# Kernel optimization log

Hardware: AMD Instinct MI355X
Metric: run time of the kernel (lower is better)

The kernel has to match this reference:

```python
import jax, jax.numpy as jnp
import numpy as np

B, H, L, D = 1, 8, 2048, 64
DP = 3   # positional coord dim
RE = 1   # extra relative features appended via concat
F = DP + RE  # LazyLinear in-features


def setup_inputs() -> dict:
    key = jax.random.key(0)
    ks = jax.random.split(key, 12)
    return {
        "q": jax.random.normal(ks[0], (B, H, L, D), jnp.float32),
        "k": jax.random.normal(ks[1], (B, H, L, D), jnp.float32),
        "v": jax.random.normal(ks[2], (B, H, L, D), jnp.float32),
        "c": jax.random.uniform(ks[3], (B, 1, 1, L), jnp.float32),
        "d_q": jax.random.normal(ks[4], (B, L, DP), jnp.float32),
        "d_k_top": jax.random.normal(ks[5], (B, L, DP), jnp.float32),
        "d_k_bot": jax.random.normal(ks[6], (B, L, DP), jnp.float32),
        "d_k_score": jax.random.uniform(ks[7], (B, L, 2, F), jnp.float32),
        "relative_top": jax.random.normal(ks[8], (B, L, L, RE), jnp.float32),
        "relative_bottom": jax.random.normal(ks[9], (B, L, L, RE), jnp.float32),
        "W_w": jax.random.normal(ks[10], (F, H), jnp.float32) * 0.1,
        "W_b": jax.random.normal(ks[11], (F, H), jnp.float32) * 0.1,
    }


def _pairwise_diff(a, b):
    # a: [B,Lq,Dp], b: [B,Lk,Dp] -> [B,Lq,Lk,Dp]
    return a[:, :, None, :] - b[:, None, :, :]


def reference(q, k, v, c, d_q, d_k_top, d_k_bot, d_k_score,
              relative_top, relative_bottom, W_w, W_b):
    # score function: scaled dot product -> [B,H,Lq,Lk]
    scores = jnp.einsum('bhqd,bhkd->bhqk', q, k) * (q.shape[-1] ** -0.5)

    # relative-position bias path
    dt = jnp.concatenate([_pairwise_diff(d_q, d_k_top), relative_top], axis=-1)     # [B,Lq,Lk,F]
    db = jnp.concatenate([_pairwise_diff(d_q, d_k_bot), relative_bottom], axis=-1)  # [B,Lq,Lk,F]
    dm = jnp.stack([dt, db], axis=3)                 # [B,Lq,Lk,2,F]
    dm = dm * d_k_score[:, None]                     # broadcast over Lq
    dm = dm.sum(axis=3)                              # [B,Lq,Lk,F]

    w = jax.nn.softplus(dm @ W_w).transpose(0, 3, 1, 2)  # [B,H,Lq,Lk]
    b = (dm @ W_b).transpose(0, 3, 1, 2)                 # [B,H,Lq,Lk]
    scores = scores * w + b

    # leaky probability function: softmax gated by per-key sampling weights c
    probs = jax.nn.softmax(scores, axis=-1) * c      # [B,H,Lq,Lk]

    out = jnp.einsum('bhqk,bhkd->bhqd', probs, v)
    return out, probs
```

## Files before the change

### kernel.cpp

```cpp
#include <hip/hip_runtime.h>
#include <cstdint>
#include <cstddef>

#define NH 8
#define LQ 2048
#define DH 64
#define NKT_HALF 16

typedef __attribute__((ext_vector_type(8))) __bf16 bf16x8;
typedef __attribute__((ext_vector_type(8))) unsigned short ushort8;
typedef __attribute__((ext_vector_type(4))) float floatx4;

__device__ __forceinline__ unsigned short bf_trunc(float x) {
    return (unsigned short)(__float_as_uint(x) >> 16);
}
__device__ __forceinline__ float bf_up(unsigned short h) {
    return __uint_as_float(((unsigned int)h) << 16);
}
__device__ __forceinline__ unsigned short bf_rne(float x) {
    unsigned int u = __float_as_uint(x);
    return (unsigned short)((u + 0x7FFFu + ((u >> 16) & 1u)) >> 16);
}
struct hl_t { unsigned short h, l; };
__device__ __forceinline__ hl_t split2(float x) {
    hl_t r;
    r.h = bf_trunc(x);
    r.l = bf_trunc(x - bf_up(r.h));
    return r;
}

#define MFMA16(A, B, C) __builtin_amdgcn_mfma_f32_16x16x32_bf16((A), (B), (C), 0, 0, 0)

__global__ __launch_bounds__(256) void prep_kernel(
    const float* __restrict__ kp,  const float* __restrict__ vp,
    const float* __restrict__ cp,  const float* __restrict__ dktp,
    const float* __restrict__ dkbp,const float* __restrict__ dksp,
    const float* __restrict__ Wwp, const float* __restrict__ Wbp,
    unsigned short* __restrict__ khig, unsigned short* __restrict__ klog,
    unsigned short* __restrict__ vhig, unsigned short* __restrict__ vlog,
    float* __restrict__ metag)
{
    const int bid = blockIdx.x;
    const int t   = threadIdx.x;

    if (bid < 256) {
        const int h = bid >> 5, kt = bid & 31;
        const int row = t >> 2, s = t & 3;
        const size_t kg = (size_t)(h * LQ) + kt * 64 + row;
        const float* src = kp + kg * DH + s * 16;
        unsigned short* dh_ = khig + kg * DH + s * 16;
        unsigned short* dl_ = klog + kg * DH + s * 16;
        ushort8 vh0, vh1, vl0, vl1;
#pragma unroll
        for (int j = 0; j < 2; ++j) {
            float4 x = *(const float4*)(src + 4 * j);
            hl_t a = split2(x.x * 0.125f), b = split2(x.y * 0.125f);
            hl_t c = split2(x.z * 0.125f), d = split2(x.w * 0.125f);
            vh0[4*j+0]=a.h; vl0[4*j+0]=a.l; vh0[4*j+1]=b.h; vl0[4*j+1]=b.l;
            vh0[4*j+2]=c.h; vl0[4*j+2]=c.l; vh0[4*j+3]=d.h; vl0[4*j+3]=d.l;
        }
#pragma unroll
        for (int j = 0; j < 2; ++j) {
            float4 x = *(const float4*)(src + 8 + 4 * j);
            hl_t a = split2(x.x * 0.125f), b = split2(x.y * 0.125f);
            hl_t c = split2(x.z * 0.125f), d = split2(x.w * 0.125f);
            vh1[4*j+0]=a.h; vl1[4*j+0]=a.l; vh1[4*j+1]=b.h; vl1[4*j+1]=b.l;
            vh1[4*j+2]=c.h; vl1[4*j+2]=c.l; vh1[4*j+3]=d.h; vl1[4*j+3]=d.l;
        }
        *(ushort8*)&dh_[0] = vh0; *(ushort8*)&dh_[8] = vh1;
        *(ushort8*)&dl_[0] = vl0; *(ushort8*)&dl_[8] = vl1;
    } else if (bid < 512) {
        const int h = (bid - 256) >> 5, kt = (bid - 256) & 31;
        const int p = t >> 4, mm = t & 15;
        const int k0 = kt * 64;
#pragma unroll
        for (int g = 0; g < 2; ++g) {
            const int kka = 2 * p + 32 * g;
            const float ca = cp[k0 + kka], cb = cp[k0 + kka + 1];
            const float* va = vp + ((size_t)(h * LQ + k0 + kka)) * DH;
            const float* vb = va + DH;
#pragma unroll
            for (int dd = 0; dd < 4; ++dd) {
                const int d = mm + 16 * dd;
                hl_t xa = split2(va[d] * ca);
                hl_t xb = split2(vb[d] * cb);
                const size_t base = ((size_t)(h * 32 + kt) * 64 + d) * 64 + kka;
                *(unsigned int*)&vhig[base] = (unsigned int)xa.h | ((unsigned int)xb.h << 16);
                *(unsigned int*)&vlog[base] = (unsigned int)xa.l | ((unsigned int)xb.l << 16);
            }
        }
    } else {
        const int idx = (bid - 512) * 256 + t;
        const int h  = idx >> 11;
        const int kg = idx & 2047;
        float Ww[4], Wb[4];
#pragma unroll
        for (int f = 0; f < 4; ++f) { Ww[f] = Wwp[f * NH + h]; Wb[f] = Wbp[f * NH + h]; }
        const float* sc_ = dksp + (size_t)kg * 8;
        const float* tp  = dktp + (size_t)kg * 3;
        const float* bt  = dkbp + (size_t)kg * 3;
        float* mo = metag + ((size_t)(h * LQ) + kg) * 12;
        float cw = 0.f, cb2 = 0.f;
#pragma unroll
        for (int f = 0; f < 3; ++f) {
            const float stf = sc_[f], sbf = sc_[4 + f];
            const float A  = stf + sbf;
            const float Bv = tp[f] * stf + bt[f] * sbf;
            mo[f]     = A * Ww[f];
            mo[4 + f] = A * Wb[f];
            cw  -= Bv * Ww[f];
            cb2 -= Bv * Wb[f];
        }
        mo[3]  = cw;              mo[7]  = cb2;
        mo[8]  = sc_[3] * Ww[3];  mo[9]  = sc_[7] * Ww[3];
        mo[10] = sc_[3] * Wb[3];  mo[11] = sc_[7] * Wb[3];
    }
}

__global__ __launch_bounds__(256, 2) void attn_main(
    const float* __restrict__ qp,  const float* __restrict__ dqp,
    const float* __restrict__ rtp, const float* __restrict__ rbp,
    const unsigned short* __restrict__ khig, const unsigned short* __restrict__ klog,
    const unsigned short* __restrict__ vhig, const unsigned short* __restrict__ vlog,
    const float* __restrict__ metag,
    float* __restrict__ probp, float* __restrict__ lws, float* __restrict__ pvws)
{
    __shared__ unsigned short sh_khi[64 * 72];
    __shared__ unsigned short sh_klo[64 * 72];
    __shared__ unsigned short sh_vhi[64 * 72];
    __shared__ unsigned short sh_vlo[64 * 72];
    __shared__ float sh_meta[64 * 12];
    __shared__ float sh_dqs[64 * 3];

    const int bid  = blockIdx.x;
    const int half = bid & 1;
    const int h    = (bid >> 1) & 7;
    const int qt   = bid >> 4;
    const int q0   = qt * 64;
    const int t    = threadIdx.x;
    const int lane = t & 63;
    const int m    = lane & 15;
    const int quad = lane >> 4;
    const int w16  = (t >> 6) * 16;

    const int srow = t >> 2, ss = t & 3;
    const int sbase = srow * 72 + ss * 16;
    const int mk = t / 3, mj = t - mk * 3;

    size_t kgb = ((size_t)(h * LQ) + half * NKT_HALF * 64 + srow) * DH + ss * 16;
    size_t vgb = ((size_t)(h * 32 + half * NKT_HALF) * 64 + srow) * 64 + ss * 16;
    size_t mgb = ((size_t)(h * LQ) + half * NKT_HALF * 64 + mk) * 12 + mj * 4;

    ushort8 rkh0 = *(const ushort8*)&khig[kgb];
    ushort8 rkh1 = *(const ushort8*)&khig[kgb + 8];
    ushort8 rkl0 = *(const ushort8*)&klog[kgb];
    ushort8 rkl1 = *(const ushort8*)&klog[kgb + 8];
    ushort8 rvh0 = *(const ushort8*)&vhig[vgb];
    ushort8 rvh1 = *(const ushort8*)&vhig[vgb + 8];
    ushort8 rvl0 = *(const ushort8*)&vlog[vgb];
    ushort8 rvl1 = *(const ushort8*)&vlog[vgb + 8];
    float4  rmeta;
    if (t < 192) rmeta = *(const float4*)&metag[mgb];

    {
        const float* src = qp + ((size_t)(h * LQ + q0 + srow)) * DH + ss * 16;
        ushort8 vh0, vh1, vl0, vl1;
#pragma unroll
        for (int j = 0; j < 2; ++j) {
            float4 x = *(const float4*)(src + 4 * j);
            hl_t a = split2(x.x), b = split2(x.y), c = split2(x.z), d = split2(x.w);
            vh0[4*j+0]=a.h; vl0[4*j+0]=a.l; vh0[4*j+1]=b.h; vl0[4*j+1]=b.l;
            vh0[4*j+2]=c.h; vl0[4*j+2]=c.l; vh0[4*j+3]=d.h; vl0[4*j+3]=d.l;
        }
#pragma unroll
        for (int j = 0; j < 2; ++j) {
            float4 x = *(const float4*)(src + 8 + 4 * j);
            hl_t a = split2(x.x), b = split2(x.y), c = split2(x.z), d = split2(x.w);
            vh1[4*j+0]=a.h; vl1[4*j+0]=a.l; vh1[4*j+1]=b.h; vl1[4*j+1]=b.l;
            vh1[4*j+2]=c.h; vl1[4*j+2]=c.l; vh1[4*j+3]=d.h; vl1[4*j+3]=d.l;
        }
        *(ushort8*)&sh_khi[sbase] = vh0;  *(ushort8*)&sh_khi[sbase + 8] = vh1;
        *(ushort8*)&sh_klo[sbase] = vl0;  *(ushort8*)&sh_klo[sbase + 8] = vl1;
        if (t < 64) {
            sh_dqs[t * 3 + 0] = dqp[(q0 + t) * 3 + 0];
            sh_dqs[t * 3 + 1] = dqp[(q0 + t) * 3 + 1];
            sh_dqs[t * 3 + 2] = dqp[(q0 + t) * 3 + 2];
        }
    }
    __syncthreads();

    bf16x8 aqh[2], aql[2];
#pragma unroll
    for (int kc = 0; kc < 2; ++kc) {
        aqh[kc] = *(const bf16x8*)&sh_khi[(w16 + m) * 72 + kc * 32 + quad * 8];
        aql[kc] = *(const bf16x8*)&sh_klo[(w16 + m) * 72 + kc * 32 + quad * 8];
    }
    float dq0[4], dq1[4], dq2[4];
#pragma unroll
    for (int r = 0; r < 4; ++r) {
        const int row = w16 + quad * 4 + r;
        dq0[r] = sh_dqs[row * 3 + 0]; dq1[r] = sh_dqs[row * 3 + 1]; dq2[r] = sh_dqs[row * 3 + 2];
    }
    __syncthreads();

    const floatx4 zf = {0.f, 0.f, 0.f, 0.f};
    floatx4 pacc[4] = {zf, zf, zf, zf};
    float lpart[4] = {0.f, 0.f, 0.f, 0.f};

    for (int kth = 0; kth < NKT_HALF; ++kth) {
        const int k0 = (half * NKT_HALF + kth) * 64;

        *(ushort8*)&sh_khi[sbase]     = rkh0;
        *(ushort8*)&sh_khi[sbase + 8] = rkh1;
        *(ushort8*)&sh_klo[sbase]     = rkl0;
        *(ushort8*)&sh_klo[sbase + 8] = rkl1;
        *(ushort8*)&sh_vhi[sbase]     = rvh0;
        *(ushort8*)&sh_vhi[sbase + 8] = rvh1;
        *(ushort8*)&sh_vlo[sbase]     = rvl0;
        *(ushort8*)&sh_vlo[sbase + 8] = rvl1;
        if (t < 192) *(float4*)&sh_meta[mk * 12 + mj * 4] = rmeta;
        __syncthreads();

        if (kth + 1 < NKT_HALF) {
            kgb += (size_t)64 * DH;
            vgb += (size_t)64 * 64;
            mgb += (size_t)64 * 12;
            rkh0 = *(const ushort8*)&khig[kgb];
            rkh1 = *(const ushort8*)&khig[kgb + 8];
            rkl0 = *(const ushort8*)&klog[kgb];
            rkl1 = *(const ushort8*)&klog[kgb + 8];
            rvh0 = *(const ushort8*)&vhig[vgb];
            rvh1 = *(const ushort8*)&vhig[vgb + 8];
            rvl0 = *(const ushort8*)&vlog[vgb];
            rvl1 = *(const ushort8*)&vlog[vgb + 8];
            if (t < 192) rmeta = *(const float4*)&metag[mgb];
        }

        float rt_[4][4], rb_[4][4];
#pragma unroll
        for (int r = 0; r < 4; ++r) {
            const size_t q = (size_t)(q0 + w16 + quad * 4 + r);
#pragma unroll
            for (int nt = 0; nt < 4; ++nt) {
                rt_[nt][r] = rtp[q * LQ + k0 + nt * 16 + m];
                rb_[nt][r] = rbp[q * LQ + k0 + nt * 16 + m];
            }
        }

        floatx4 sc[4] = {zf, zf, zf, zf};
#pragma unroll
        for (int nt = 0; nt < 4; ++nt) {
#pragma unroll
            for (int kc = 0; kc < 2; ++kc) {
                const int kb = (nt * 16 + m) * 72 + kc * 32 + quad * 8;
                bf16x8 bh = *(const bf16x8*)&sh_khi[kb];
                bf16x8 bl = *(const bf16x8*)&sh_klo[kb];
                sc[nt] = MFMA16(aqh[kc], bh, sc[nt]);
                sc[nt] = MFMA16(aql[kc], bh, sc[nt]);
                sc[nt] = MFMA16(aqh[kc], bl, sc[nt]);
            }
        }
        __syncthreads();

        unsigned short* ebf = sh_klo;
#pragma unroll
        for (int nt = 0; nt < 4; ++nt) {
            const int kcol = nt * 16 + m;
            const float m0 = sh_meta[kcol * 12 + 0],  m1 = sh_meta[kcol * 12 + 1];
            const float m2 = sh_meta[kcol * 12 + 2],  m3 = sh_meta[kcol * 12 + 3];
            const float m4 = sh_meta[kcol * 12 + 4],  m5 = sh_meta[kcol * 12 + 5];
            const float m6 = sh_meta[kcol * 12 + 6],  m7 = sh_meta[kcol * 12 + 7];
            const float m8 = sh_meta[kcol * 12 + 8],  m9 = sh_meta[kcol * 12 + 9];
            const float mA = sh_meta[kcol * 12 + 10], mB = sh_meta[kcol * 12 + 11];
#pragma unroll
            for (int r = 0; r < 4; ++r) {
                float ww = fmaf(dq0[r], m0, m3); ww = fmaf(dq1[r], m1, ww); ww = fmaf(dq2[r], m2, ww);
                ww = fmaf(rt_[nt][r], m8, ww);   ww = fmaf(rb_[nt][r], m9, ww);
                float bb = fmaf(dq0[r], m4, m7); bb = fmaf(dq1[r], m5, bb); bb = fmaf(dq2[r], m6, bb);
                bb = fmaf(rt_[nt][r], mA, bb);   bb = fmaf(rb_[nt][r], mB, bb);
                const float wg = fmaxf(ww, 0.f) + __logf(1.f + __expf(-fabsf(ww)));
                const float sv = fmaf(sc[nt][r], wg, bb);
                const float e  = __expf(sv - 8.0f);
                lpart[r] += e;
                probp[((size_t)(h * LQ + q0 + w16 + quad * 4 + r)) * LQ + k0 + kcol] = e;
                ebf[(w16 + quad * 4 + r) * 72 + kcol] = bf_rne(e);
            }
        }

        bf16x8 ap0 = *(const bf16x8*)&ebf[(w16 + m) * 72 + quad * 8];
        bf16x8 ap1 = *(const bf16x8*)&ebf[(w16 + m) * 72 + 32 + quad * 8];
#pragma unroll
        for (int nt = 0; nt < 4; ++nt) {
            const int vb = (nt * 16 + m) * 72 + quad * 8;
            bf16x8 bh0 = *(const bf16x8*)&sh_vhi[vb];
            bf16x8 bl0 = *(const bf16x8*)&sh_vlo[vb];
            bf16x8 bh1 = *(const bf16x8*)&sh_vhi[vb + 32];
            bf16x8 bl1 = *(const bf16x8*)&sh_vlo[vb + 32];
            pacc[nt] = MFMA16(ap0, bh0, pacc[nt]);
            pacc[nt] = MFMA16(ap0, bl0, pacc[nt]);
            pacc[nt] = MFMA16(ap1, bh1, pacc[nt]);
            pacc[nt] = MFMA16(ap1, bl1, pacc[nt]);
        }
        __syncthreads();
    }

#pragma unroll
    for (int off = 1; off < 16; off <<= 1) {
#pragma unroll
        for (int r = 0; r < 4; ++r) lpart[r] += __shfl_xor(lpart[r], off, 64);
    }
    if (m == 0) {
#pragma unroll
        for (int r = 0; r < 4; ++r)
            lws[half * (NH * LQ) + h * LQ + q0 + w16 + quad * 4 + r] = lpart[r];
    }
#pragma unroll
    for (int nt = 0; nt < 4; ++nt) {
#pragma unroll
        for (int r = 0; r < 4; ++r) {
            const size_t row = (size_t)(h * LQ + q0 + w16 + quad * 4 + r);
            pvws[(size_t)half * (NH * LQ * DH) + row * DH + nt * 16 + m] = pacc[nt][r];
        }
    }
}

__global__ __launch_bounds__(256) void norm_combine(
    float* __restrict__ probp, const float* __restrict__ cp,
    const float* __restrict__ lws, const float* __restrict__ pvws,
    float* __restrict__ outp)
{
    __shared__ float rl8[8];
    const int t    = threadIdx.x;
    const int row0 = blockIdx.x * 8;
    const float4 c0 = *(const float4*)(cp + t * 4);
    const float4 c1 = *(const float4*)(cp + (t + 256) * 4);
    if (t < 8) rl8[t] = 1.0f / (lws[row0 + t] + lws[NH * LQ + row0 + t]);
    __syncthreads();
#pragma unroll 2
    for (int rr = 0; rr < 8; ++rr) {
        const float rl = rl8[rr];
        float* p = probp + (size_t)(row0 + rr) * LQ;
        float4 x0 = *(const float4*)(p + t * 4);
        float4 x1 = *(const float4*)(p + (t + 256) * 4);
        x0.x *= rl * c0.x; x0.y *= rl * c0.y; x0.z *= rl * c0.z; x0.w *= rl * c0.w;
        x1.x *= rl * c1.x; x1.y *= rl * c1.y; x1.z *= rl * c1.z; x1.w *= rl * c1.w;
        *(float4*)(p + t * 4)         = x0;
        *(float4*)(p + (t + 256) * 4) = x1;
    }
#pragma unroll
    for (int j = 0; j < 2; ++j) {
        const int lin = j * 256 + t;
        const int rr  = lin >> 6, d = lin & 63;
        const size_t rowd = (size_t)(row0 + rr) * DH + d;
        outp[rowd] = (pvws[rowd] + pvws[(size_t)(NH * LQ * DH) + rowd]) * rl8[rr];
    }
}

extern "C" void kernel_launch(void* const* d_in, const int* in_sizes, int n_in,
                              void* d_out, int out_size, void* d_ws, size_t ws_size,
                              hipStream_t stream)
{
    (void)in_sizes; (void)n_in; (void)out_size; (void)ws_size;
    const float* qp   = (const float*)d_in[0];
    const float* kp   = (const float*)d_in[1];
    const float* vp   = (const float*)d_in[2];
    const float* cp   = (const float*)d_in[3];
    const float* dqp  = (const float*)d_in[4];
    const float* dktp = (const float*)d_in[5];
    const float* dkbp = (const float*)d_in[6];
    const float* dksp = (const float*)d_in[7];
    const float* rtp  = (const float*)d_in[8];
    const float* rbp  = (const float*)d_in[9];
    const float* Wwp  = (const float*)d_in[10];
    const float* Wbp  = (const float*)d_in[11];

    float* outp  = (float*)d_out;
    float* probp = (float*)d_out + (size_t)NH * LQ * DH;

    float* lws  = (float*)d_ws;
    float* pvws = lws + 2 * (NH * LQ);
    unsigned short* khig = (unsigned short*)(pvws + (size_t)2 * NH * LQ * DH);
    unsigned short* klog = khig + (size_t)NH * LQ * DH;
    unsigned short* vhig = klog + (size_t)NH * LQ * DH;
    unsigned short* vlog = vhig + (size_t)NH * LQ * DH;
    float* metag = (float*)(vlog + (size_t)NH * LQ * DH);

    prep_kernel<<<dim3(576), dim3(256), 0, stream>>>(
        kp, vp, cp, dktp, dkbp, dksp, Wwp, Wbp, khig, klog, vhig, vlog, metag);
    attn_main<<<dim3(512), dim3(256), 0, stream>>>(
        qp, dqp, rtp, rbp, khig, klog, vhig, vlog, metag, probp, lws, pvws);
    norm_combine<<<dim3(2048), dim3(256), 0, stream>>>(probp, cp, lws, pvws, outp);
}
```

Before: 286.2 us.

## Double-buffer K/V tiles in LDS via async global-to-LDS loads with swizzle

Replaces register-staged K/V/meta prefetch with direct global_load_lds DMA into a double-buffered LDS tile. The prep kernel now writes K, V and meta in a per-tile XOR-swizzled layout so the copies can be straight 16-byte chunks. The probability tile gets its own LDS buffer, which removes one barrier per iteration. This aims to cut register pressure and LDS store work, and to overlap the next tile's load with compute. In exchange LDS use roughly doubles, which risks occupancy, and correctness depends on the DMA completing before the barrier.

```diff
diff --git a/kernel.cpp b/kernel.cpp
--- a/kernel.cpp
+++ b/kernel.cpp
@@ -30,6 +30,12 @@
 }
 
 #define MFMA16(A, B, C) __builtin_amdgcn_mfma_f32_16x16x32_bf16((A), (B), (C), 0, 0, 0)
+
+__device__ __forceinline__ void gl16(const void* g, void* l) {
+    __builtin_amdgcn_global_load_lds(
+        (const __attribute__((address_space(1))) void*)g,
+        (__attribute__((address_space(3))) void*)l, 16, 0, 0);
+}
 
 __global__ __launch_bounds__(256) void prep_kernel(
     const float* __restrict__ kp,  const float* __restrict__ vp,
@@ -48,8 +54,6 @@
         const int row = t >> 2, s = t & 3;
         const size_t kg = (size_t)(h * LQ) + kt * 64 + row;
         const float* src = kp + kg * DH + s * 16;
-        unsigned short* dh_ = khig + kg * DH + s * 16;
-        unsigned short* dl_ = klog + kg * DH + s * 16;
         ushort8 vh0, vh1, vl0, vl1;
 #pragma unroll
         for (int j = 0; j < 2; ++j) {
@@ -67,12 +71,17 @@
             vh1[4*j+0]=a.h; vl1[4*j+0]=a.l; vh1[4*j+1]=b.h; vl1[4*j+1]=b.l;
             vh1[4*j+2]=c.h; vl1[4*j+2]=c.l; vh1[4*j+3]=d.h; vl1[4*j+3]=d.l;
         }
-        *(ushort8*)&dh_[0] = vh0; *(ushort8*)&dh_[8] = vh1;
-        *(ushort8*)&dl_[0] = vl0; *(ushort8*)&dl_[8] = vl1;
+        const size_t tb = (size_t)(h * 32 + kt) * 4096;
+        const int swz = (row & 7) << 3;
+        const int o1 = (row * 64 + s * 16) ^ swz;
+        const int o2 = (row * 64 + s * 16 + 8) ^ swz;
+        *(ushort8*)&khig[tb + o1] = vh0; *(ushort8*)&khig[tb + o2] = vh1;
+        *(ushort8*)&klog[tb + o1] = vl0; *(ushort8*)&klog[tb + o2] = vl1;
     } else if (bid < 512) {
         const int h = (bid - 256) >> 5, kt = (bid - 256) & 31;
         const int p = t >> 4, mm = t & 15;
         const int k0 = kt * 64;
+        const size_t tb = (size_t)(h * 32 + kt) * 4096;
 #pragma unroll
         for (int g = 0; g < 2; ++g) {
             const int kka = 2 * p + 32 * g;
@@ -84,9 +93,9 @@
                 const int d = mm + 16 * dd;
                 hl_t xa = split2(va[d] * ca);
                 hl_t xb = split2(vb[d] * cb);
-                const size_t base = ((size_t)(h * 32 + kt) * 64 + d) * 64 + kka;
-                *(unsigned int*)&vhig[base] = (unsigned int)xa.h | ((unsigned int)xb.h << 16);
-                *(unsigned int*)&vlog[base] = (unsigned int)xa.l | ((unsigned int)xb.l << 16);
+                const int e = (d * 64 + kka) ^ ((d & 7) << 3);
+                *(unsigned int*)&vhig[tb + e] = (unsigned int)xa.h | ((unsigned int)xb.h << 16);
+                *(unsigned int*)&vlog[tb + e] = (unsigned int)xa.l | ((unsigned int)xb.l << 16);
             }
         }
     } else {
@@ -99,7 +108,7 @@
         const float* sc_ = dksp + (size_t)kg * 8;
         const float* tp  = dktp + (size_t)kg * 3;
         const float* bt  = dkbp + (size_t)kg * 3;
-        float* mo = metag + ((size_t)(h * LQ) + kg) * 12;
+        float* mo = metag + ((size_t)(h * 32 + (kg >> 6)) * 64 + (kg & 63)) * 12;
         float cw = 0.f, cb2 = 0.f;
 #pragma unroll
         for (int f = 0; f < 3; ++f) {
@@ -117,6 +126,28 @@
     }
 }
 
+#define DMA_KV(BUF, TILE)                                                      \
+    {                                                                          \
+        const size_t gtb_ = (size_t)(TILE) * 4096;                             \
+        const size_t mtb_ = (size_t)(TILE) * 768;                              \
+        const int wo_ = w * 1024;                                              \
+        gl16(&khig[gtb_ + wo_ + le],       &sh_buf[BUF][0][wo_]);              \
+        gl16(&khig[gtb_ + wo_ + 512 + le], &sh_buf[BUF][0][wo_ + 512]);        \
+        gl16(&klog[gtb_ + wo_ + le],       &sh_buf[BUF][1][wo_]);              \
+        gl16(&klog[gtb_ + wo_ + 512 + le], &sh_buf[BUF][1][wo_ + 512]);        \
+        gl16(&vhig[gtb_ + wo_ + le],       &sh_buf[BUF][2][wo_]);              \
+        gl16(&vhig[gtb_ + wo_ + 512 + le], &sh_buf[BUF][2][wo_ + 512]);        \
+        gl16(&vlog[gtb_ + wo_ + le],       &sh_buf[BUF][3][wo_]);              \
+        gl16(&vlog[gtb_ + wo_ + 512 + le], &sh_buf[BUF][3][wo_ + 512]);        \
+        if (w == 0) {                                                          \
+            gl16(&metag[mtb_ + lf],       &sh_meta2[BUF][0]);                  \
+            gl16(&metag[mtb_ + 256 + lf], &sh_meta2[BUF][256]);                \
+            gl16(&metag[mtb_ + 512 + lf], &sh_meta2[BUF][512]);                \
+        }                                                                      \
+    }
+
+#define SWZ8(e, row) ((e) ^ (((row) & 7) << 3))
+
 __global__ __launch_bounds__(256, 2) void attn_main(
     const float* __restrict__ qp,  const float* __restrict__ dqp,
     const float* __restrict__ rtp, const float* __restrict__ rbp,
@@ -125,11 +156,9 @@
     const float* __restrict__ metag,
     float* __restrict__ probp, float* __restrict__ lws, float* __restrict__ pvws)
 {
-    __shared__ unsigned short sh_khi[64 * 72];
-    __shared__ unsigned short sh_klo[64 * 72];
-    __shared__ unsigned short sh_vhi[64 * 72];
-    __shared__ unsigned short sh_vlo[64 * 72];
-    __shared__ float sh_meta[64 * 12];
+    __shared__ unsigned short sh_buf[2][4][4096];
+    __shared__ float sh_meta2[2][768];
+    __shared__ unsigned short sh_ebf[64 * 72];
     __shared__ float sh_dqs[64 * 3];
 
     const int bid  = blockIdx.x;
@@ -142,27 +171,16 @@
     const int m    = lane & 15;
     const int quad = lane >> 4;
     const int w16  = (t >> 6) * 16;
-
-    const int srow = t >> 2, ss = t & 3;
-    const int sbase = srow * 72 + ss * 16;
-    const int mk = t / 3, mj = t - mk * 3;
-
-    size_t kgb = ((size_t)(h * LQ) + half * NKT_HALF * 64 + srow) * DH + ss * 16;
-    size_t vgb = ((size_t)(h * 32 + half * NKT_HALF) * 64 + srow) * 64 + ss * 16;
-    size_t mgb = ((size_t)(h * LQ) + half * NKT_HALF * 64 + mk) * 12 + mj * 4;
-
-    ushort8 rkh0 = *(const ushort8*)&khig[kgb];
-    ushort8 rkh1 = *(const ushort8*)&khig[kgb + 8];
-    ushort8 rkl0 = *(const ushort8*)&klog[kgb];
-    ushort8 rkl1 = *(const ushort8*)&klog[kgb + 8];
-    ushort8 rvh0 = *(const ushort8*)&vhig[vgb];
-    ushort8 rvh1 = *(const ushort8*)&vhig[vgb + 8];
-    ushort8 rvl0 = *(const ushort8*)&vlog[vgb];
-    ushort8 rvl1 = *(const ushort8*)&vlog[vgb + 8];
-    float4  rmeta;
-    if (t < 192) rmeta = *(const float4*)&metag[mgb];
+    const int w    = t >> 6;
+    const int le   = lane * 8;
+    const int lf   = lane * 4;
+
+    const int tile0 = h * 32 + half * NKT_HALF;
+
+    DMA_KV(0, tile0);
 
     {
+        const int srow = t >> 2, ss = t & 3;
         const float* src = qp + ((size_t)(h * LQ + q0 + srow)) * DH + ss * 16;
         ushort8 vh0, vh1, vl0, vl1;
 #pragma unroll
@@ -179,8 +197,10 @@
             vh1[4*j+0]=a.h; vl1[4*j+0]=a.l; vh1[4*j+1]=b.h; vl1[4*j+1]=b.l;
             vh1[4*j+2]=c.h; vl1[4*j+2]=c.l; vh1[4*j+3]=d.h; vl1[4*j+3]=d.l;
         }
-        *(ushort8*)&sh_khi[sbase] = vh0;  *(ushort8*)&sh_khi[sbase + 8] = vh1;
-        *(ushort8*)&sh_klo[sbase] = vl0;  *(ushort8*)&sh_klo[sbase + 8] = vl1;
+        const int o1 = SWZ8(srow * 64 + ss * 16, srow);
+        const int o2 = SWZ8(srow * 64 + ss * 16 + 8, srow);
+        *(ushort8*)&sh_buf[1][0][o1] = vh0;  *(ushort8*)&sh_buf[1][0][o2] = vh1;
+        *(ushort8*)&sh_buf[1][1][o1] = vl0;  *(ushort8*)&sh_buf[1][1][o2] = vl1;
         if (t < 64) {
             sh_dqs[t * 3 + 0] = dqp[(q0 + t) * 3 + 0];
             sh_dqs[t * 3 + 1] = dqp[(q0 + t) * 3 + 1];
@@ -190,10 +210,14 @@
     __syncthreads();
 
     bf16x8 aqh[2], aql[2];
-#pragma unroll
-    for (int kc = 0; kc < 2; ++kc) {
-        aqh[kc] = *(const bf16x8*)&sh_khi[(w16 + m) * 72 + kc * 32 + quad * 8];
-        aql[kc] = *(const bf16x8*)&sh_klo[(w16 + m) * 72 + kc * 32 + quad * 8];
+    {
+        const int qrow = w16 + m;
+#pragma unroll
+        for (int kc = 0; kc < 2; ++kc) {
+            const int qo = SWZ8(qrow * 64 + kc * 32 + quad * 8, qrow);
+            aqh[kc] = *(const bf16x8*)&sh_buf[1][0][qo];
+            aql[kc] = *(const bf16x8*)&sh_buf[1][1][qo];
+        }
     }
     float dq0[4], dq1[4], dq2[4];
 #pragma unroll
@@ -208,33 +232,8 @@
     float lpart[4] = {0.f, 0.f, 0.f, 0.f};
 
     for (int kth = 0; kth < NKT_HALF; ++kth) {
-        const int k0 = (half * NKT_HALF + kth) * 64;
-
-        *(ushort8*)&sh_khi[sbase]     = rkh0;
-        *(ushort8*)&sh_khi[sbase + 8] = rkh1;
-        *(ushort8*)&sh_klo[sbase]     = rkl0;
-        *(ushort8*)&sh_klo[sbase + 8] = rkl1;
-        *(ushort8*)&sh_vhi[sbase]     = rvh0;
-        *(ushort8*)&sh_vhi[sbase + 8] = rvh1;
-        *(ushort8*)&sh_vlo[sbase]     = rvl0;
-        *(ushort8*)&sh_vlo[sbase + 8] = rvl1;
-        if (t < 192) *(float4*)&sh_meta[mk * 12 + mj * 4] = rmeta;
-        __syncthreads();
-
-        if (kth + 1 < NKT_HALF) {
-            kgb += (size_t)64 * DH;
-            vgb += (size_t)64 * 64;
-            mgb += (size_t)64 * 12;
-            rkh0 = *(const ushort8*)&khig[kgb];
-            rkh1 = *(const ushort8*)&khig[kgb + 8];
-            rkl0 = *(const ushort8*)&klog[kgb];
-            rkl1 = *(const ushort8*)&klog[kgb + 8];
-            rvh0 = *(const ushort8*)&vhig[vgb];
-            rvh1 = *(const ushort8*)&vhig[vgb + 8];
-            rvl0 = *(const ushort8*)&vlog[vgb];
-            rvl1 = *(const ushort8*)&vlog[vgb + 8];
-            if (t < 192) rmeta = *(const float4*)&metag[mgb];
-        }
+        const int cur = kth & 1;
+        const int k0  = (half * NKT_HALF + kth) * 64;
 
         float rt_[4][4], rb_[4][4];
 #pragma unroll
@@ -247,31 +246,35 @@
             }
         }
 
+        if (kth + 1 < NKT_HALF) {
+            DMA_KV(cur ^ 1, tile0 + kth + 1);
+        }
+
         floatx4 sc[4] = {zf, zf, zf, zf};
 #pragma unroll
         for (int nt = 0; nt < 4; ++nt) {
+            const int row = nt * 16 + m;
 #pragma unroll
             for (int kc = 0; kc < 2; ++kc) {
-                const int kb = (nt * 16 + m) * 72 + kc * 32 + quad * 8;
-                bf16x8 bh = *(const bf16x8*)&sh_khi[kb];
-                bf16x8 bl = *(const bf16x8*)&sh_klo[kb];
+                const int kb = SWZ8(row * 64 + kc * 32 + quad * 8, row);
+                bf16x8 bh = *(const bf16x8*)&sh_buf[cur][0][kb];
+                bf16x8 bl = *(const bf16x8*)&sh_buf[cur][1][kb];
                 sc[nt] = MFMA16(aqh[kc], bh, sc[nt]);
                 sc[nt] = MFMA16(aql[kc], bh, sc[nt]);
                 sc[nt] = MFMA16(aqh[kc], bl, sc[nt]);
             }
         }
-        __syncthreads();
-
-        unsigned short* ebf = sh_klo;
+
+        const float* mt = sh_meta2[cur];
 #pragma unroll
         for (int nt = 0; nt < 4; ++nt) {
             const int kcol = nt * 16 + m;
-            const float m0 = sh_meta[kcol * 12 + 0],  m1 = sh_meta[kcol * 12 + 1];
-            const float m2 = sh_meta[kcol * 12 + 2],  m3 = sh_meta[kcol * 12 + 3];
-            const float m4 = sh_meta[kcol * 12 + 4],  m5 = sh_meta[kcol * 12 + 5];
-            const float m6 = sh_meta[kcol * 12 + 6],  m7 = sh_meta[kcol * 12 + 7];
-            const float m8 = sh_meta[kcol * 12 + 8],  m9 = sh_meta[kcol * 12 + 9];
-            const float mA = sh_meta[kcol * 12 + 10], mB = sh_meta[kcol * 12 + 11];
+            const float m0 = mt[kcol * 12 + 0],  m1 = mt[kcol * 12 + 1];
+            const float m2 = mt[kcol * 12 + 2],  m3 = mt[kcol * 12 + 3];
+            const float m4 = mt[kcol * 12 + 4],  m5 = mt[kcol * 12 + 5];
+            const float m6 = mt[kcol * 12 + 6],  m7 = mt[kcol * 12 + 7];
+            const float m8 = mt[kcol * 12 + 8],  m9 = mt[kcol * 12 + 9];
+            const float mA = mt[kcol * 12 + 10], mB = mt[kcol * 12 + 11];
 #pragma unroll
             for (int r = 0; r < 4; ++r) {
                 float ww = fmaf(dq0[r], m0, m3); ww = fmaf(dq1[r], m1, ww); ww = fmaf(dq2[r], m2, ww);
@@ -283,24 +286,27 @@
                 const float e  = __expf(sv - 8.0f);
                 lpart[r] += e;
                 probp[((size_t)(h * LQ + q0 + w16 + quad * 4 + r)) * LQ + k0 + kcol] = e;
-                ebf[(w16 + quad * 4 + r) * 72 + kcol] = bf_rne(e);
+                sh_ebf[(w16 + quad * 4 + r) * 72 + kcol] = bf_rne(e);
             }
         }
 
-        bf16x8 ap0 = *(const bf16x8*)&ebf[(w16 + m) * 72 + quad * 8];
-        bf16x8 ap1 = *(const bf16x8*)&ebf[(w16 + m) * 72 + 32 + quad * 8];
+        bf16x8 ap0 = *(const bf16x8*)&sh_ebf[(w16 + m) * 72 + quad * 8];
+        bf16x8 ap1 = *(const bf16x8*)&sh_ebf[(w16 + m) * 72 + 32 + quad * 8];
 #pragma unroll
         for (int nt = 0; nt < 4; ++nt) {
-            const int vb = (nt * 16 + m) * 72 + quad * 8;
-            bf16x8 bh0 = *(const bf16x8*)&sh_vhi[vb];
-            bf16x8 bl0 = *(const bf16x8*)&sh_vlo[vb];
-            bf16x8 bh1 = *(const bf16x8*)&sh_vhi[vb + 32];
-            bf16x8 bl1 = *(const bf16x8*)&sh_vlo[vb + 32];
+            const int vrow = nt * 16 + m;
+            const int vb0 = SWZ8(vrow * 64 + quad * 8, vrow);
+            const int vb1 = SWZ8(vrow * 64 + 32 + quad * 8, vrow);
+            bf16x8 bh0 = *(const bf16x8*)&sh_buf[cur][2][vb0];
+            bf16x8 bl0 = *(const bf16x8*)&sh_buf[cur][3][vb0];
+            bf16x8 bh1 = *(const bf16x8*)&sh_buf[cur][2][vb1];
+            bf16x8 bl1 = *(const bf16x8*)&sh_buf[cur][3][vb1];
             pacc[nt] = MFMA16(ap0, bh0, pacc[nt]);
             pacc[nt] = MFMA16(ap0, bl0, pacc[nt]);
             pacc[nt] = MFMA16(ap1, bh1, pacc[nt]);
             pacc[nt] = MFMA16(ap1, bl1, pacc[nt]);
         }
+
         __syncthreads();
     }
 
```

Result: no change. 289.1 us (+1.0%).
